# Performance work log

Hardware: AMD Instinct MI355X
Metric: run time of the kernel (lower is better)

The kernel has to match this reference:

```python
import jax, jax.numpy as jnp
import numpy as np

L = 5        # num_layer
D = 128      # emb_dim
N = 100000   # nodes
E = 500000   # edges
G = 128      # graphs in batch
NUM_TYPES = 100
NUM_ATTRS = 1000
MAX_DEPTH = 21


def _bn(x, g, b):
    # training-mode BatchNorm1d statistics (per-feature over rows)
    mu = x.mean(axis=0)
    var = x.var(axis=0)
    return (x - mu) * jax.lax.rsqrt(var + 1e-5) * g + b


def setup_inputs() -> dict:
    key = jax.random.key(0)
    ks = jax.random.split(key, 24)
    inp = {}
    x0 = jax.random.randint(ks[0], (N,), 0, NUM_TYPES)
    x1 = jax.random.randint(ks[1], (N,), 0, NUM_ATTRS)
    inp['x'] = jnp.stack([x0, x1], axis=1)
    inp['node_depth'] = jax.random.randint(ks[2], (N,), 0, MAX_DEPTH)
    inp['edge_index'] = jax.random.randint(ks[3], (2, E), 0, N)
    inp['batch'] = jnp.sort(jax.random.randint(ks[4], (N,), 0, G))
    inp['edge_attr'] = jax.random.normal(ks[5], (E, 2), dtype=jnp.float32)
    s = 0.02
    inp['type_emb'] = jax.random.normal(ks[6], (NUM_TYPES, D), dtype=jnp.float32) * s
    inp['attr_emb'] = jax.random.normal(ks[7], (NUM_ATTRS, D), dtype=jnp.float32) * s
    inp['depth_emb'] = jax.random.normal(ks[8], (MAX_DEPTH, D), dtype=jnp.float32) * s
    inp['vn_emb'] = jnp.zeros((1, D), dtype=jnp.float32)  # init constant 0
    inp['eps'] = jnp.zeros((L,), dtype=jnp.float32)       # GIN eps
    inp['edge_W'] = jax.random.normal(ks[9], (L, 2, D), dtype=jnp.float32) * s
    inp['edge_b'] = jnp.zeros((L, D), dtype=jnp.float32)
    inp['gin_W1'] = jax.random.normal(ks[10], (L, D, 2 * D), dtype=jnp.float32) * s
    inp['gin_b1'] = jnp.zeros((L, 2 * D), dtype=jnp.float32)
    inp['gin_bng'] = jnp.ones((L, 2 * D), dtype=jnp.float32)
    inp['gin_bnb'] = jnp.zeros((L, 2 * D), dtype=jnp.float32)
    inp['gin_W2'] = jax.random.normal(ks[11], (L, 2 * D, D), dtype=jnp.float32) * s
    inp['gin_b2'] = jnp.zeros((L, D), dtype=jnp.float32)
    inp['bng'] = jnp.ones((L, D), dtype=jnp.float32)
    inp['bnb'] = jnp.zeros((L, D), dtype=jnp.float32)
    inp['vn_W1'] = jax.random.normal(ks[12], (L - 1, D, 2 * D), dtype=jnp.float32) * s
    inp['vn_b1'] = jnp.zeros((L - 1, 2 * D), dtype=jnp.float32)
    inp['vn_bn1g'] = jnp.ones((L - 1, 2 * D), dtype=jnp.float32)
    inp['vn_bn1b'] = jnp.zeros((L - 1, 2 * D), dtype=jnp.float32)
    inp['vn_W2'] = jax.random.normal(ks[13], (L - 1, 2 * D, D), dtype=jnp.float32) * s
    inp['vn_b2'] = jnp.zeros((L - 1, D), dtype=jnp.float32)
    inp['vn_bn2g'] = jnp.ones((L - 1, D), dtype=jnp.float32)
    inp['vn_bn2b'] = jnp.zeros((L - 1, D), dtype=jnp.float32)
    return inp


def reference(x, node_depth, edge_index, batch, edge_attr,
              type_emb, attr_emb, depth_emb, vn_emb, eps,
              edge_W, edge_b, gin_W1, gin_b1, gin_bng, gin_bnb, gin_W2, gin_b2,
              bng, bnb, vn_W1, vn_b1, vn_bn1g, vn_bn1b, vn_W2, vn_b2, vn_bn2g, vn_bn2b):
    # node encoder: type + attribute + depth embeddings  -> [N, D]
    h = type_emb[x[:, 0]] + attr_emb[x[:, 1]] + depth_emb[node_depth]
    vn = jnp.broadcast_to(vn_emb[0], (G, D))  # virtual node per graph
    src, dst = edge_index[0], edge_index[1]
    for l in range(L):
        # broadcast virtual node to its graph's nodes
        h = h + vn[batch]
        # GIN conv: aggr_j relu(h_j + edge_emb), then (1+eps)*h + aggr -> MLP
        eemb = edge_attr @ edge_W[l] + edge_b[l]            # [E, D]
        msg = jax.nn.relu(h[src] + eemb)                    # [E, D]
        aggr = jax.ops.segment_sum(msg, dst, num_segments=N)
        z = (1.0 + eps[l]) * h + aggr
        z = jax.nn.relu(_bn(z @ gin_W1[l] + gin_b1[l], gin_bng[l], gin_bnb[l]))
        z = z @ gin_W2[l] + gin_b2[l]
        hn = _bn(z, bng[l], bnb[l])                         # outer BatchNorm
        if l < L - 1:
            hn = jax.nn.relu(hn)                            # dropout=identity (eval)
            # virtual node update: global_add_pool of pre-conv h + MLP
            vt = jax.ops.segment_sum(h, batch, num_segments=G) + vn
            vt = jax.nn.relu(_bn(vt @ vn_W1[l] + vn_b1[l], vn_bn1g[l], vn_bn1b[l]))
            vn = jax.nn.relu(_bn(vt @ vn_W2[l] + vn_b2[l], vn_bn2g[l], vn_bn2b[l]))
        h = hn
    return h  # JK == 'last'
```

## Files before the change

### kernel.cpp

```cpp
#include <hip/hip_runtime.h>

#define D 128
#define GG 128
#define SLOTS 64

typedef __attribute__((ext_vector_type(8))) short bf16x8;
typedef __attribute__((ext_vector_type(4))) float f32x4;

__device__ __forceinline__ short f2bf(float f) {
  unsigned u = __float_as_uint(f);
  unsigned r = u + 0x7fffu + ((u >> 16) & 1u);
  return (short)(r >> 16);
}
__device__ __forceinline__ float bf2f(unsigned short h) {
  return __uint_as_float(((unsigned)h) << 16);
}

__device__ __forceinline__ void bn_coef(float s, float q, float invn, float g, float b,
                                        float& sc, float& sh) {
  float mu = s * invn;
  float var = q * invn - mu * mu;
  sc = g * rsqrtf(var + 1e-5f);
  sh = b - mu * sc;
}

__global__ void k_deg(int E, const int* __restrict__ dst, int* __restrict__ deg) {
  int e = blockIdx.x * 256 + threadIdx.x;
  if (e < E) atomicAdd(&deg[dst[e]], 1);
}

__global__ void k_scan1(int N, const int* __restrict__ deg,
                        int* __restrict__ incl, int* __restrict__ blksum) {
  __shared__ int s[256];
  int t = threadIdx.x, n = blockIdx.x * 256 + t;
  int v = (n < N) ? ((deg[n] + 3) & ~3) : 0;
  s[t] = v; __syncthreads();
  for (int off = 1; off < 256; off <<= 1) {
    int x = (t >= off) ? s[t - off] : 0;
    __syncthreads();
    s[t] += x;
    __syncthreads();
  }
  if (n < N) incl[n] = s[t];
  if (t == 255) blksum[blockIdx.x] = s[255];
}

__global__ void k_scan2(int B, int* __restrict__ blksum) {
  __shared__ int s[512];
  int t = threadIdx.x;
  s[t] = (t < B) ? blksum[t] : 0;
  __syncthreads();
  for (int off = 1; off < 512; off <<= 1) {
    int x = (t >= off) ? s[t - off] : 0;
    __syncthreads();
    s[t] += x;
    __syncthreads();
  }
  if (t < B) blksum[t] = s[t];
}

__global__ void k_scan3(int N, const int* __restrict__ incl, const int* __restrict__ blksum,
                        const int* __restrict__ deg, int* __restrict__ row_ptr) {
  int n = blockIdx.x * 256 + threadIdx.x;
  if (n >= N) return;
  int b = n >> 8;
  int off = (b > 0) ? blksum[b - 1] : 0;
  int pdeg = (deg[n] + 3) & ~3;
  row_ptr[n] = off + incl[n] - pdeg;
  if (n == N - 1) row_ptr[N] = off + incl[n];
}

__global__ void k_fill(int E, const int* __restrict__ src, const int* __restrict__ dst,
                       const float* __restrict__ ea, const int* __restrict__ row_ptr,
                       int* __restrict__ cursor, int4* __restrict__ er) {
  int e = blockIdx.x * 256 + threadIdx.x;
  if (e >= E) return;
  int d = dst[e];
  int pos = row_ptr[d] + atomicAdd(&cursor[d], 1);
  er[pos] = make_int4(src[e] << 8, __float_as_int(ea[2 * e]), __float_as_int(ea[2 * e + 1]), 0);
}

__global__ void k_padfill(int N, const int* __restrict__ deg, const int* __restrict__ row_ptr,
                          int4* __restrict__ er) {
  int n = blockIdx.x * 256 + threadIdx.x;
  if (n >= N) return;
  int s = row_ptr[n] + deg[n], e = row_ptr[n + 1];
  int4 pad = make_int4(N << 8, 0, 0, 0);
  for (int p = s; p < e; ++p) er[p] = pad;
}

__global__ void k_sentinel(int N, short* __restrict__ h2) {
  h2[(size_t)N * D + threadIdx.x] = f2bf(-1e30f);
}

__global__ void k_pack(const float* __restrict__ gW1, const float* __restrict__ gW2,
                       short* __restrict__ w1t, short* __restrict__ w2t) {
  int id = blockIdx.x * 256 + threadIdx.x;
  if (id < 5 * 256 * 128) {
    int l = id / 32768, r = id % 32768, n = r / 128, k = r % 128;
    w1t[id] = f2bf(gW1[l * 32768 + k * 256 + n]);
  }
  if (id < 5 * 128 * 256) {
    int l = id / 32768, r = id % 32768, n = r / 256, k = r % 256;
    w2t[id] = f2bf(gW2[l * 32768 + k * 128 + n]);
  }
}

__global__ void k_coef(int NC,
                       const float* __restrict__ part_s, const float* __restrict__ part_q,
                       float* __restrict__ outs, float* __restrict__ outq) {
  int t = threadIdx.x;
  if (t >= NC) return;
  float s = 0.f, q = 0.f;
  #pragma unroll 4
  for (int i = 0; i < SLOTS; ++i) {
    s += part_s[i * NC + t];
    q += part_q[i * NC + t];
  }
  outs[t] = s; outq[t] = q;
}

__global__ void k_nodeprep(int N, int mode,
    const int* __restrict__ x, const int* __restrict__ depth,
    const float* __restrict__ te, const float* __restrict__ ae, const float* __restrict__ de,
    const short* __restrict__ z2, const float* __restrict__ s2, const float* __restrict__ q2,
    const float* __restrict__ g2, const float* __restrict__ b2,
    int vn_mode, const float* __restrict__ vne,
    const float* __restrict__ t2v, const float* __restrict__ vs2, const float* __restrict__ vq2,
    const float* __restrict__ vg2, const float* __restrict__ vb2,
    const int* __restrict__ batch,
    short* __restrict__ h2, float* __restrict__ vt_pool, int do_pool)
{
  int t = threadIdx.x;
  int d = t & (D - 1);
  int lane = t >> 7;
  int n0 = blockIdx.x * 16;
  float invn = 1.0f / (float)N;
  float sc = 0.f, sh = 0.f, vsc = 0.f, vsh = 0.f;
  if (mode == 1)    bn_coef(s2[d], q2[d], invn, g2[d], b2[d], sc, sh);
  if (vn_mode == 1) bn_coef(vs2[d], vq2[d], 1.0f / (float)GG, vg2[d], vb2[d], vsc, vsh);
  int cur = -1; float acc = 0.f;
  for (int k = 0; k < 8; ++k) {
    int n = n0 + lane * 8 + k;
    if (n >= N) break;
    float hv;
    if (mode == 0) {
      hv = te[x[2 * n] * D + d] + ae[x[2 * n + 1] * D + d] + de[depth[n] * D + d];
    } else {
      float z = bf2f((unsigned short)z2[(size_t)n * D + d]);
      hv = fmaxf(z * sc + sh, 0.f);
    }
    int g = batch[n];
    float vnv;
    if (vn_mode == 0) vnv = vne[d];
    else { float tv = t2v[g * D + d]; vnv = fmaxf(tv * vsc + vsh, 0.f); }
    float h = hv + vnv;
    h2[(size_t)n * D + d] = f2bf(h);
    if (do_pool) {
      if (g != cur) {
        if (cur >= 0) atomicAdd(&vt_pool[cur * D + d], acc);
        cur = g; acc = 0.f;
      }
      acc += h;
    }
  }
  if (do_pool && cur >= 0) atomicAdd(&vt_pool[cur * D + d], acc);
}

__global__ void __launch_bounds__(256) k_gather(int N,
    const int* __restrict__ row_ptr, const int4* __restrict__ er,
    const float* __restrict__ ew, const float* __restrict__ eb,
    const float* __restrict__ epsp,
    const short* __restrict__ h2, short* __restrict__ am)
{
  int t = threadIdx.x;
  int w = t >> 6, l = t & 63;
  int n = blockIdx.x * 4 + w;
  if (n >= N) return;
  const char* h2b = (const char*)h2;
  int lb = l << 2;
  int d0 = l * 2;
  float ew00 = ew[d0], ew01 = ew[d0 + 1];
  float ew10 = ew[D + d0], ew11 = ew[D + d0 + 1];
  float eb0 = eb[d0], eb1 = eb[d0 + 1];
  float ep1 = 1.0f + epsp[0];
  unsigned hv = *(const unsigned*)(h2b + ((size_t)n << 8) + lb);
  float acc0 = ep1 * bf2f((unsigned short)(hv & 0xffff));
  float acc1 = ep1 * bf2f((unsigned short)(hv >> 16));
  int beg = row_ptr[n], end = row_ptr[n + 1];
  for (int i = beg; i < end; i += 4) {
    int4 e0 = er[i], e1 = er[i + 1], e2 = er[i + 2], e3 = er[i + 3];
    unsigned v0 = *(const unsigned*)(h2b + e0.x + lb);
    unsigned v1 = *(const unsigned*)(h2b + e1.x + lb);
    unsigned v2 = *(const unsigned*)(h2b + e2.x + lb);
    unsigned v3 = *(const unsigned*)(h2b + e3.x + lb);
    float a0x = __int_as_float(e0.y), a0y = __int_as_float(e0.z);
    float a1x = __int_as_float(e1.y), a1y = __int_as_float(e1.z);
    float a2x = __int_as_float(e2.y), a2y = __int_as_float(e2.z);
    float a3x = __int_as_float(e3.y), a3y = __int_as_float(e3.z);
    acc0 += fmaxf(bf2f((unsigned short)(v0 & 0xffff)) + a0x * ew00 + a0y * ew10 + eb0, 0.f);
    acc1 += fmaxf(bf2f((unsigned short)(v0 >> 16))    + a0x * ew01 + a0y * ew11 + eb1, 0.f);
    acc0 += fmaxf(bf2f((unsigned short)(v1 & 0xffff)) + a1x * ew00 + a1y * ew10 + eb0, 0.f);
    acc1 += fmaxf(bf2f((unsigned short)(v1 >> 16))    + a1x * ew01 + a1y * ew11 + eb1, 0.f);
    acc0 += fmaxf(bf2f((unsigned short)(v2 & 0xffff)) + a2x * ew00 + a2y * ew10 + eb0, 0.f);
    acc1 += fmaxf(bf2f((unsigned short)(v2 >> 16))    + a2x * ew01 + a2y * ew11 + eb1, 0.f);
    acc0 += fmaxf(bf2f((unsigned short)(v3 & 0xffff)) + a3x * ew00 + a3y * ew10 + eb0, 0.f);
    acc1 += fmaxf(bf2f((unsigned short)(v3 >> 16))    + a3x * ew01 + a3y * ew11 + eb1, 0.f);
  }
  unsigned o = ((unsigned)(unsigned short)f2bf(acc0)) |
               (((unsigned)(unsigned short)f2bf(acc1)) << 16);
  *(unsigned*)(am + (size_t)n * D + d0) = o;
}

template<int STAGES, int BN_A>
__global__ void __launch_bounds__(256, 2) k_gemm(int N, int NC, float invn,
    const short* __restrict__ A, int strideA,
    const short* __restrict__ Bt, int strideB,
    const float* __restrict__ bias,
    const float* __restrict__ pAs, const float* __restrict__ pAq,
    const float* __restrict__ g1, const float* __restrict__ b1,
    short* __restrict__ C, int strideC,
    float* __restrict__ part_s, float* __restrict__ part_q)
{
  __shared__ __align__(16) char As[32768];
  __shared__ __align__(16) char Bs[32768];
  __shared__ float scs[256], shs[256];
  __shared__ float cs[128], cq[128];
  int t = threadIdx.x;
  int m0 = blockIdx.x * 128;
  int n0 = blockIdx.y * 128;
  int w = t >> 6, l = t & 63;
  int wr = w >> 1, wc = w & 1;
  int lm = l & 15, kb = l >> 4;

  if (t < 128) { cs[t] = 0.f; cq[t] = 0.f; }
  if (BN_A) {
    float s = 0.f, q = 0.f;
    #pragma unroll 4
    for (int i = 0; i < SLOTS; ++i) {
      s += pAs[i * 256 + t];
      q += pAq[i * 256 + t];
    }
    float a, c;
    bn_coef(s, q, invn, g1[t], b1[t], a, c);
    scs[t] = a; shs[t] = c;
  }
  __syncthreads();

  f32x4 acc[4][4];
  #pragma unroll
  for (int j = 0; j < 4; ++j) {
    float bj = bias[n0 + wc * 64 + j * 16 + lm];
    #pragma unroll
    for (int i = 0; i < 4; ++i) acc[i][j] = (f32x4){bj, bj, bj, bj};
  }

  #pragma unroll
  for (int s = 0; s < STAGES; ++s) {
    if (s > 0) __syncthreads();
    #pragma unroll
    for (int r = 0; r < 8; ++r) {
      int p = (r * 256 + t) * 16;
      int row = p >> 8, c = p & 255;
      int gr = m0 + row; if (gr > N - 1) gr = N - 1;
      bf16x8 v = *(const bf16x8*)((const char*)A + (size_t)gr * strideA + s * 256 + c);
      if (BN_A) {
        int kg = s * 128 + (c >> 1);
        float4 s0 = *(const float4*)(scs + kg);
        float4 s1 = *(const float4*)(scs + kg + 4);
        float4 h0 = *(const float4*)(shs + kg);
        float4 h1 = *(const float4*)(shs + kg + 4);
        v[0] = f2bf(fmaxf(bf2f((unsigned short)v[0]) * s0.x + h0.x, 0.f));
        v[1] = f2bf(fmaxf(bf2f((unsigned short)v[1]) * s0.y + h0.y, 0.f));
        v[2] = f2bf(fmaxf(bf2f((unsigned short)v[2]) * s0.z + h0.z, 0.f));
        v[3] = f2bf(fmaxf(bf2f((unsigned short)v[3]) * s0.w + h0.w, 0.f));
        v[4] = f2bf(fmaxf(bf2f((unsigned short)v[4]) * s1.x + h1.x, 0.f));
        v[5] = f2bf(fmaxf(bf2f((unsigned short)v[5]) * s1.y + h1.y, 0.f));
        v[6] = f2bf(fmaxf(bf2f((unsigned short)v[6]) * s1.z + h1.z, 0.f));
        v[7] = f2bf(fmaxf(bf2f((unsigned short)v[7]) * s1.w + h1.w, 0.f));
      }
      *(bf16x8*)(As + row * 256 + (c ^ ((row & 7) << 4))) = v;
    }
    #pragma unroll
    for (int r = 0; r < 8; ++r) {
      int p = (r * 256 + t) * 16;
      int col = p >> 8, c = p & 255;
      bf16x8 v = *(const bf16x8*)((const char*)Bt + (size_t)(n0 + col) * strideB + s * 256 + c);
      *(bf16x8*)(Bs + col * 256 + (c ^ ((col & 7) << 4))) = v;
    }
    __syncthreads();
    #pragma unroll
    for (int ks = 0; ks < 4; ++ks) {
      int kB = ks * 64 + kb * 16;
      bf16x8 fa[4], fb[4];
      #pragma unroll
      for (int i = 0; i < 4; ++i) {
        int rl = wr * 64 + i * 16 + lm;
        fa[i] = *(const bf16x8*)(As + rl * 256 + (kB ^ ((rl & 7) << 4)));
      }
      #pragma unroll
      for (int j = 0; j < 4; ++j) {
        int cl = wc * 64 + j * 16 + lm;
        fb[j] = *(const bf16x8*)(Bs + cl * 256 + (kB ^ ((cl & 7) << 4)));
      }
      #pragma unroll
      for (int i = 0; i < 4; ++i)
        #pragma unroll
        for (int j = 0; j < 4; ++j)
          acc[i][j] = __builtin_amdgcn_mfma_f32_16x16x32_bf16(fa[i], fb[j], acc[i][j], 0, 0, 0);
    }
  }

  #pragma unroll
  for (int j = 0; j < 4; ++j) {
    int col = n0 + wc * 64 + j * 16 + lm;
    float sv = 0.f, qv = 0.f;
    #pragma unroll
    for (int i = 0; i < 4; ++i) {
      #pragma unroll
      for (int r = 0; r < 4; ++r) {
        int row = m0 + wr * 64 + i * 16 + kb * 4 + r;
        float vv = acc[i][j][r];
        if (row < N) { C[(size_t)row * strideC + col] = f2bf(vv); sv += vv; qv += vv * vv; }
      }
    }
    sv += __shfl_xor(sv, 16); sv += __shfl_xor(sv, 32);
    qv += __shfl_xor(qv, 16); qv += __shfl_xor(qv, 32);
    if (l < 16) { atomicAdd(&cs[col - n0], sv); atomicAdd(&cq[col - n0], qv); }
  }
  __syncthreads();
  if (t < 128) {
    int slot = (blockIdx.x + blockIdx.y) & (SLOTS - 1);
    atomicAdd(&part_s[(size_t)slot * NC + n0 + t], cs[t]);
    atomicAdd(&part_q[(size_t)slot * NC + n0 + t], cq[t]);
  }
}

__global__ void k_vn1(const float* __restrict__ vt_pool,
    int vn_mode, const float* __restrict__ vne, const float* __restrict__ t2v,
    const float* __restrict__ vs2, const float* __restrict__ vq2,
    const float* __restrict__ vg2, const float* __restrict__ vb2,
    const float* __restrict__ W1, const float* __restrict__ b1,
    float* __restrict__ t1v, float* __restrict__ s1, float* __restrict__ q1)
{
  __shared__ float vrow[128];
  int g = blockIdx.x, t = threadIdx.x;
  if (t < 128) {
    float vnv;
    if (vn_mode == 0) vnv = vne[t];
    else {
      float sc, sh;
      bn_coef(vs2[t], vq2[t], 1.f / (float)GG, vg2[t], vb2[t], sc, sh);
      vnv = fmaxf(t2v[g * D + t] * sc + sh, 0.f);
    }
    vrow[t] = vt_pool[g * D + t] + vnv;
  }
  __syncthreads();
  float acc = b1[t];
  for (int k = 0; k < 128; ++k) acc += vrow[k] * W1[k * 256 + t];
  t1v[g * 256 + t] = acc;
  atomicAdd(&s1[t], acc);
  atomicAdd(&q1[t], acc * acc);
}

__global__ void k_vn2(const float* __restrict__ t1v,
    const float* __restrict__ s1, const float* __restrict__ q1,
    const float* __restrict__ g1, const float* __restrict__ b1bn,
    const float* __restrict__ W2, const float* __restrict__ b2,
    float* __restrict__ t2v, float* __restrict__ s2, float* __restrict__ q2)
{
  __shared__ float p[256];
  int g = blockIdx.x, t = threadIdx.x;
  for (int u = t; u < 256; u += 128) {
    float sc, sh;
    bn_coef(s1[u], q1[u], 1.f / (float)GG, g1[u], b1bn[u], sc, sh);
    p[u] = fmaxf(t1v[g * 256 + u] * sc + sh, 0.f);
  }
  __syncthreads();
  float acc = b2[t];
  for (int k = 0; k < 256; ++k) acc += p[k] * W2[k * D + t];
  t2v[g * D + t] = acc;
  atomicAdd(&s2[t], acc);
  atomicAdd(&q2[t], acc * acc);
}

__global__ void k_out(int N, const short* __restrict__ z2,
    const float* __restrict__ s2, const float* __restrict__ q2,
    const float* __restrict__ g2, const float* __restrict__ b2, float* __restrict__ out)
{
  long long idx = (long long)blockIdx.x * 256 + threadIdx.x;
  long long base = idx * 2;
  if (base >= (long long)N * D) return;
  int d = (int)(base & (D - 1));
  float invn = 1.f / (float)N;
  unsigned v = *(const unsigned*)(z2 + base);
  float sc0, sh0, sc1, sh1;
  bn_coef(s2[d], q2[d], invn, g2[d], b2[d], sc0, sh0);
  bn_coef(s2[d + 1], q2[d + 1], invn, g2[d + 1], b2[d + 1], sc1, sh1);
  out[base]     = bf2f((unsigned short)(v & 0xffff)) * sc0 + sh0;
  out[base + 1] = bf2f((unsigned short)(v >> 16))    * sc1 + sh1;
}

extern "C" void kernel_launch(void* const* d_in, const int* in_sizes, int n_in,
                              void* d_out, int out_size, void* d_ws, size_t ws_size,
                              hipStream_t stream) {
  const int*   x     = (const int*)d_in[0];
  const int*   depth = (const int*)d_in[1];
  const int*   eidx  = (const int*)d_in[2];
  const int*   batch = (const int*)d_in[3];
  const float* ea    = (const float*)d_in[4];
  const float* te    = (const float*)d_in[5];
  const float* aemb  = (const float*)d_in[6];
  const float* de    = (const float*)d_in[7];
  const float* vne   = (const float*)d_in[8];
  const float* epsp  = (const float*)d_in[9];
  const float* eW    = (const float*)d_in[10];
  const float* eb    = (const float*)d_in[11];
  const float* gW1   = (const float*)d_in[12];
  const float* gb1   = (const float*)d_in[13];
  const float* gbng  = (const float*)d_in[14];
  const float* gbnb  = (const float*)d_in[15];
  const float* gW2   = (const float*)d_in[16];
  const float* gb2   = (const float*)d_in[17];
  const float* bng   = (const float*)d_in[18];
  const float* bnb   = (const float*)d_in[19];
  const float* vW1   = (const float*)d_in[20];
  const float* vb1   = (const float*)d_in[21];
  const float* vbn1g = (const float*)d_in[22];
  const float* vbn1b = (const float*)d_in[23];
  const float* vW2   = (const float*)d_in[24];
  const float* vb2   = (const float*)d_in[25];
  const float* vbn2g = (const float*)d_in[26];
  const float* vbn2b = (const float*)d_in[27];

  int N = in_sizes[0] / 2;
  int E = in_sizes[2] / 2;
  const int* src = eidx;
  const int* dst = eidx + E;

  char* wsp = (char*)d_ws;
  auto alloc = [&](size_t bytes) -> char* {
    char* p = wsp; wsp += (bytes + 15) & ~(size_t)15; return p;
  };
  short* h2         = (short*)alloc((size_t)(N + 1) * 128 * 2);
  short* am         = (short*)alloc((size_t)N * 128 * 2);
  short* t1         = (short*)alloc((size_t)N * 256 * 2);
  short* z2         = (short*)alloc((size_t)N * 128 * 2);
  short* w1t        = (short*)alloc((size_t)5 * 256 * 128 * 2);
  short* w2t        = (short*)alloc((size_t)5 * 128 * 256 * 2);
  int*   row_ptr    = (int*)alloc((size_t)(N + 1) * 4);
  int*   incl       = (int*)alloc((size_t)N * 4);
  int*   blksum     = (int*)alloc(512 * 4);
  int4*  er         = (int4*)alloc(((size_t)E + 3 * (size_t)N + 16) * 16);
  char* zero_base = wsp;
  int*  deg    = (int*)alloc((size_t)N * 4);
  int*  cursor = (int*)alloc((size_t)N * 4);
  float* sp = (float*)wsp;
  float *p1s[5], *p1q[5], *p2s[5], *p2q[5], *s2s[5], *q2s[5];
  for (int l = 0; l < 5; ++l) {
    p1s[l]=sp; sp+=SLOTS*256; p1q[l]=sp; sp+=SLOTS*256;
    p2s[l]=sp; sp+=SLOTS*128; p2q[l]=sp; sp+=SLOTS*128;
    s2s[l]=sp; sp+=128; q2s[l]=sp; sp+=128;
  }
  float *vt[4], *t1v[4], *t2v[4], *vs1[4], *vq1[4], *vs2[4], *vq2[4];
  for (int l = 0; l < 4; ++l) {
    vt[l]=sp;  sp+=GG*D;
    t1v[l]=sp; sp+=GG*256;
    t2v[l]=sp; sp+=GG*D;
    vs1[l]=sp; sp+=256; vq1[l]=sp; sp+=256;
    vs2[l]=sp; sp+=128; vq2[l]=sp; sp+=128;
  }
  size_t zero_bytes = (size_t)((char*)sp - zero_base);
  hipMemsetAsync(zero_base, 0, zero_bytes, stream);

  int eblk = (E + 255) / 256;
  int nblk = (N + 255) / 256;
  int B = nblk;
  k_deg<<<eblk, 256, 0, stream>>>(E, dst, deg);
  k_scan1<<<nblk, 256, 0, stream>>>(N, deg, incl, blksum);
  k_scan2<<<1, 512, 0, stream>>>(B, blksum);
  k_scan3<<<nblk, 256, 0, stream>>>(N, incl, blksum, deg, row_ptr);
  k_fill<<<eblk, 256, 0, stream>>>(E, src, dst, ea, row_ptr, cursor, er);
  k_padfill<<<nblk, 256, 0, stream>>>(N, deg, row_ptr, er);
  k_sentinel<<<1, 128, 0, stream>>>(N, h2);

  k_pack<<<(5 * 256 * 128 + 255) / 256, 256, 0, stream>>>(gW1, gW2, w1t, w2t);

  int nblk_a = (N + 15) / 16;
  int nblk_gth = (N + 3) / 4;
  int nblk_m = (N + 127) / 128;
  float invn = 1.f / (float)N;

  for (int l = 0; l < 5; ++l) {
    int mode    = (l == 0) ? 0 : 1;
    int vn_mode = (l == 0) ? 0 : 1;
    int do_pool = (l < 4) ? 1 : 0;
    const float* ps2  = (l > 0) ? s2s[l-1] : s2s[0];
    const float* pq2  = (l > 0) ? q2s[l-1] : q2s[0];
    const float* pg2  = (l > 0) ? bng + (l-1)*D : bng;
    const float* pb2  = (l > 0) ? bnb + (l-1)*D : bnb;
    const float* pt2v = (l > 0) ? t2v[l-1] : t2v[0];
    const float* pvs2 = (l > 0) ? vs2[l-1] : vs2[0];
    const float* pvq2 = (l > 0) ? vq2[l-1] : vq2[0];
    const float* pvg2 = (l > 0) ? vbn2g + (l-1)*D : vbn2g;
    const float* pvb2 = (l > 0) ? vbn2b + (l-1)*D : vbn2b;

    k_nodeprep<<<nblk_a, 256, 0, stream>>>(N, mode, x, depth, te, aemb, de,
        z2, ps2, pq2, pg2, pb2,
        vn_mode, vne, pt2v, pvs2, pvq2, pvg2, pvb2,
        batch, h2, do_pool ? vt[l] : vt[0], do_pool);

    k_gather<<<nblk_gth, 256, 0, stream>>>(N, row_ptr, er,
        eW + l*2*D, eb + l*D, epsp + l, h2, am);

    k_gemm<1, 0><<<dim3(nblk_m, 2), 256, 0, stream>>>(N, 256, invn,
        am, 256, w1t + (size_t)l*256*128, 256,
        gb1 + l*256, nullptr, nullptr, nullptr, nullptr,
        t1, 256, p1s[l], p1q[l]);

    k_gemm<2, 1><<<dim3(nblk_m, 1), 256, 0, stream>>>(N, 128, invn,
        t1, 512, w2t + (size_t)l*128*256, 512,
        gb2 + l*128, p1s[l], p1q[l], gbng + l*256, gbnb + l*256,
        z2, 128, p2s[l], p2q[l]);

    k_coef<<<1, 128, 0, stream>>>(128, p2s[l], p2q[l], s2s[l], q2s[l]);

    if (l < 4) {
      k_vn1<<<GG, 256, 0, stream>>>(vt[l], vn_mode, vne, pt2v, pvs2, pvq2, pvg2, pvb2,
          vW1 + (size_t)l*128*256, vb1 + l*256, t1v[l], vs1[l], vq1[l]);
      k_vn2<<<GG, 128, 0, stream>>>(t1v[l], vs1[l], vq1[l],
          vbn1g + l*256, vbn1b + l*256,
          vW2 + (size_t)l*256*128, vb2 + l*128, t2v[l], vs2[l], vq2[l]);
    }
  }

  k_out<<<(int)(((long long)N * D / 2 + 255) / 256), 256, 0, stream>>>(N, z2, s2s[4], q2s[4],
      bng + 4*D, bnb + 4*D, (float*)d_out);
}
```

Measured before the change: 910.2 us.

## Fold BN-stat reductions into GEMM tails and fuse virtual-node MLP kernels

Adds a last-block ticket to each GEMM so the final block reduces the per-slot partial sums and writes either BN scale/shift coefficients or the summed stats. This removes the separate k_coef launch and the 64-slot reduction every GEMM2 block used to repeat in its prologue. k_vn1 and k_vn2 are merged into one kernel that uses a grid-wide spin barrier on a counter between the two layers. This cuts per-layer launches, but the spin barrier only works if all 128 blocks are co-resident, and the ticket pattern depends on fences being correct.

```diff
diff --git a/kernel.cpp b/kernel.cpp
--- a/kernel.cpp
+++ b/kernel.cpp
@@ -104,20 +104,6 @@
     int l = id / 32768, r = id % 32768, n = r / 256, k = r % 256;
     w2t[id] = f2bf(gW2[l * 32768 + k * 128 + n]);
   }
-}
-
-__global__ void k_coef(int NC,
-                       const float* __restrict__ part_s, const float* __restrict__ part_q,
-                       float* __restrict__ outs, float* __restrict__ outq) {
-  int t = threadIdx.x;
-  if (t >= NC) return;
-  float s = 0.f, q = 0.f;
-  #pragma unroll 4
-  for (int i = 0; i < SLOTS; ++i) {
-    s += part_s[i * NC + t];
-    q += part_q[i * NC + t];
-  }
-  outs[t] = s; outq[t] = q;
 }
 
 __global__ void k_nodeprep(int N, int mode,
@@ -212,20 +198,23 @@
   *(unsigned*)(am + (size_t)n * D + d0) = o;
 }
 
-template<int STAGES, int BN_A>
+template<int STAGES, int BN_A, int FINAL>
 __global__ void __launch_bounds__(256, 2) k_gemm(int N, int NC, float invn,
     const short* __restrict__ A, int strideA,
     const short* __restrict__ Bt, int strideB,
     const float* __restrict__ bias,
-    const float* __restrict__ pAs, const float* __restrict__ pAq,
-    const float* __restrict__ g1, const float* __restrict__ b1,
+    const float* __restrict__ scA, const float* __restrict__ shA,
+    const float* __restrict__ gam, const float* __restrict__ bet,
     short* __restrict__ C, int strideC,
-    float* __restrict__ part_s, float* __restrict__ part_q)
+    float* __restrict__ part_s, float* __restrict__ part_q,
+    int* __restrict__ ticket, int ntick,
+    float* __restrict__ outA, float* __restrict__ outB)
 {
   __shared__ __align__(16) char As[32768];
   __shared__ __align__(16) char Bs[32768];
   __shared__ float scs[256], shs[256];
   __shared__ float cs[128], cq[128];
+  __shared__ bool is_last;
   int t = threadIdx.x;
   int m0 = blockIdx.x * 128;
   int n0 = blockIdx.y * 128;
@@ -234,17 +223,7 @@
   int lm = l & 15, kb = l >> 4;
 
   if (t < 128) { cs[t] = 0.f; cq[t] = 0.f; }
-  if (BN_A) {
-    float s = 0.f, q = 0.f;
-    #pragma unroll 4
-    for (int i = 0; i < SLOTS; ++i) {
-      s += pAs[i * 256 + t];
-      q += pAq[i * 256 + t];
-    }
-    float a, c;
-    bn_coef(s, q, invn, g1[t], b1[t], a, c);
-    scs[t] = a; shs[t] = c;
-  }
+  if (BN_A) { scs[t] = scA[t]; shs[t] = shA[t]; }
   __syncthreads();
 
   f32x4 acc[4][4];
@@ -334,54 +313,82 @@
     atomicAdd(&part_s[(size_t)slot * NC + n0 + t], cs[t]);
     atomicAdd(&part_q[(size_t)slot * NC + n0 + t], cq[t]);
   }
-}
-
-__global__ void k_vn1(const float* __restrict__ vt_pool,
-    int vn_mode, const float* __restrict__ vne, const float* __restrict__ t2v,
-    const float* __restrict__ vs2, const float* __restrict__ vq2,
-    const float* __restrict__ vg2, const float* __restrict__ vb2,
+  if (t == 0) {
+    __threadfence();
+    int v = atomicAdd(ticket, 1);
+    is_last = (v == ntick - 1);
+  }
+  __syncthreads();
+  if (is_last && t < NC) {
+    float s = 0.f, q = 0.f;
+    #pragma unroll 4
+    for (int i = 0; i < SLOTS; ++i) {
+      s += __hip_atomic_load(&part_s[(size_t)i * NC + t], __ATOMIC_RELAXED, __HIP_MEMORY_SCOPE_AGENT);
+      q += __hip_atomic_load(&part_q[(size_t)i * NC + t], __ATOMIC_RELAXED, __HIP_MEMORY_SCOPE_AGENT);
+    }
+    if (FINAL == 1) {
+      float a, c;
+      bn_coef(s, q, invn, gam[t], bet[t], a, c);
+      outA[t] = a; outB[t] = c;
+    } else {
+      outA[t] = s; outB[t] = q;
+    }
+  }
+}
+
+__global__ void k_vn12(const float* __restrict__ vt_pool,
+    int vn_mode, const float* __restrict__ vne, const float* __restrict__ t2v_prev,
+    const float* __restrict__ pvs2, const float* __restrict__ pvq2,
+    const float* __restrict__ pvg2, const float* __restrict__ pvb2,
     const float* __restrict__ W1, const float* __restrict__ b1,
-    float* __restrict__ t1v, float* __restrict__ s1, float* __restrict__ q1)
+    const float* __restrict__ g1bn, const float* __restrict__ b1bn,
+    const float* __restrict__ W2, const float* __restrict__ b2,
+    float* __restrict__ t2v,
+    float* __restrict__ s1, float* __restrict__ q1,
+    float* __restrict__ s2, float* __restrict__ q2,
+    int* __restrict__ cnt)
 {
   __shared__ float vrow[128];
+  __shared__ float p[256];
   int g = blockIdx.x, t = threadIdx.x;
   if (t < 128) {
     float vnv;
     if (vn_mode == 0) vnv = vne[t];
     else {
       float sc, sh;
-      bn_coef(vs2[t], vq2[t], 1.f / (float)GG, vg2[t], vb2[t], sc, sh);
-      vnv = fmaxf(t2v[g * D + t] * sc + sh, 0.f);
+      bn_coef(pvs2[t], pvq2[t], 1.f / (float)GG, pvg2[t], pvb2[t], sc, sh);
+      vnv = fmaxf(t2v_prev[g * D + t] * sc + sh, 0.f);
     }
     vrow[t] = vt_pool[g * D + t] + vnv;
   }
   __syncthreads();
-  float acc = b1[t];
-  for (int k = 0; k < 128; ++k) acc += vrow[k] * W1[k * 256 + t];
-  t1v[g * 256 + t] = acc;
-  atomicAdd(&s1[t], acc);
-  atomicAdd(&q1[t], acc * acc);
-}
-
-__global__ void k_vn2(const float* __restrict__ t1v,
-    const float* __restrict__ s1, const float* __restrict__ q1,
-    const float* __restrict__ g1, const float* __restrict__ b1bn,
-    const float* __restrict__ W2, const float* __restrict__ b2,
-    float* __restrict__ t2v, float* __restrict__ s2, float* __restrict__ q2)
-{
-  __shared__ float p[256];
-  int g = blockIdx.x, t = threadIdx.x;
-  for (int u = t; u < 256; u += 128) {
+  float acc1 = b1[t];
+  for (int k = 0; k < 128; ++k) acc1 += vrow[k] * W1[k * 256 + t];
+  atomicAdd(&s1[t], acc1);
+  atomicAdd(&q1[t], acc1 * acc1);
+  __syncthreads();
+  if (t == 0) {
+    __threadfence();
+    atomicAdd(cnt, 1);
+    while (__hip_atomic_load(cnt, __ATOMIC_ACQUIRE, __HIP_MEMORY_SCOPE_AGENT) < GG)
+      __builtin_amdgcn_s_sleep(2);
+  }
+  __syncthreads();
+  {
+    float ss = __hip_atomic_load(&s1[t], __ATOMIC_RELAXED, __HIP_MEMORY_SCOPE_AGENT);
+    float qq = __hip_atomic_load(&q1[t], __ATOMIC_RELAXED, __HIP_MEMORY_SCOPE_AGENT);
     float sc, sh;
-    bn_coef(s1[u], q1[u], 1.f / (float)GG, g1[u], b1bn[u], sc, sh);
-    p[u] = fmaxf(t1v[g * 256 + u] * sc + sh, 0.f);
-  }
-  __syncthreads();
-  float acc = b2[t];
-  for (int k = 0; k < 256; ++k) acc += p[k] * W2[k * D + t];
-  t2v[g * D + t] = acc;
-  atomicAdd(&s2[t], acc);
-  atomicAdd(&q2[t], acc * acc);
+    bn_coef(ss, qq, 1.f / (float)GG, g1bn[t], b1bn[t], sc, sh);
+    p[t] = fmaxf(acc1 * sc + sh, 0.f);
+  }
+  __syncthreads();
+  if (t < 128) {
+    float acc2 = b2[t];
+    for (int k = 0; k < 256; ++k) acc2 += p[k] * W2[k * D + t];
+    t2v[g * D + t] = acc2;
+    atomicAdd(&s2[t], acc2);
+    atomicAdd(&q2[t], acc2 * acc2);
+  }
 }
 
 __global__ void k_out(int N, const short* __restrict__ z2,
@@ -452,9 +459,13 @@
   int*   incl       = (int*)alloc((size_t)N * 4);
   int*   blksum     = (int*)alloc(512 * 4);
   int4*  er         = (int4*)alloc(((size_t)E + 3 * (size_t)N + 16) * 16);
+  float* sc1        = (float*)alloc(256 * 4);
+  float* sh1        = (float*)alloc(256 * 4);
   char* zero_base = wsp;
   int*  deg    = (int*)alloc((size_t)N * 4);
   int*  cursor = (int*)alloc((size_t)N * 4);
+  int*  tick   = (int*)alloc(16 * 4);
+  int*  vncnt  = (int*)alloc(8 * 4);
   float* sp = (float*)wsp;
   float *p1s[5], *p1q[5], *p2s[5], *p2q[5], *s2s[5], *q2s[5];
   for (int l = 0; l < 5; ++l) {
@@ -462,10 +473,9 @@
     p2s[l]=sp; sp+=SLOTS*128; p2q[l]=sp; sp+=SLOTS*128;
     s2s[l]=sp; sp+=128; q2s[l]=sp; sp+=128;
   }
-  float *vt[4], *t1v[4], *t2v[4], *vs1[4], *vq1[4], *vs2[4], *vq2[4];
+  float *vt[4], *t2v[4], *vs1[4], *vq1[4], *vs2[4], *vq2[4];
   for (int l = 0; l < 4; ++l) {
     vt[l]=sp;  sp+=GG*D;
-    t1v[l]=sp; sp+=GG*256;
     t2v[l]=sp; sp+=GG*D;
     vs1[l]=sp; sp+=256; vq1[l]=sp; sp+=256;
     vs2[l]=sp; sp+=128; vq2[l]=sp; sp+=128;
@@ -513,24 +523,23 @@
     k_gather<<<nblk_gth, 256, 0, stream>>>(N, row_ptr, er,
         eW + l*2*D, eb + l*D, epsp + l, h2, am);
 
-    k_gemm<1, 0><<<dim3(nblk_m, 2), 256, 0, stream>>>(N, 256, invn,
+    k_gemm<1, 0, 1><<<dim3(nblk_m, 2), 256, 0, stream>>>(N, 256, invn,
         am, 256, w1t + (size_t)l*256*128, 256,
-        gb1 + l*256, nullptr, nullptr, nullptr, nullptr,
-        t1, 256, p1s[l], p1q[l]);
-
-    k_gemm<2, 1><<<dim3(nblk_m, 1), 256, 0, stream>>>(N, 128, invn,
+        gb1 + l*256, nullptr, nullptr, gbng + l*256, gbnb + l*256,
+        t1, 256, p1s[l], p1q[l], tick + 2*l, nblk_m * 2, sc1, sh1);
+
+    k_gemm<2, 1, 2><<<dim3(nblk_m, 1), 256, 0, stream>>>(N, 128, invn,
         t1, 512, w2t + (size_t)l*128*256, 512,
-        gb2 + l*128, p1s[l], p1q[l], gbng + l*256, gbnb + l*256,
-        z2, 128, p2s[l], p2q[l]);
-
-    k_coef<<<1, 128, 0, stream>>>(128, p2s[l], p2q[l], s2s[l], q2s[l]);
+        gb2 + l*128, sc1, sh1, nullptr, nullptr,
+        z2, 128, p2s[l], p2q[l], tick + 2*l + 1, nblk_m, s2s[l], q2s[l]);
 
     if (l < 4) {
-      k_vn1<<<GG, 256, 0, stream>>>(vt[l], vn_mode, vne, pt2v, pvs2, pvq2, pvg2, pvb2,
-          vW1 + (size_t)l*128*256, vb1 + l*256, t1v[l], vs1[l], vq1[l]);
-      k_vn2<<<GG, 128, 0, stream>>>(t1v[l], vs1[l], vq1[l],
+      k_vn12<<<GG, 256, 0, stream>>>(vt[l], vn_mode, vne, pt2v,
+          pvs2, pvq2, pvg2, pvb2,
+          vW1 + (size_t)l*128*256, vb1 + l*256,
           vbn1g + l*256, vbn1b + l*256,
-          vW2 + (size_t)l*256*128, vb2 + l*128, t2v[l], vs2[l], vq2[l]);
+          vW2 + (size_t)l*256*128, vb2 + l*128,
+          t2v[l], vs1[l], vq1[l], vs2[l], vq2[l], vncnt + l);
     }
   }
 
```

After: 1.291 ms. +41.9%, slower.

## Read GEMM B operand directly from global, drop B LDS tile, raise occupancy

Applied to the files above, without the earlier changes.

The GEMM kernel no longer stages the weight tile in shared memory. Each wave loads its B fragments straight from global memory (weights are small and likely cache-resident), which halves LDS use so launch bounds can rise from 2 to 4 blocks per SM. The BatchNorm coefficient reduction for the second GEMM moves out of every block into a separate small k_coef launch that writes scale and shift once, so blocks no longer each re-sum 64 partial slots. The trade-off is extra global/L2 traffic for repeated B reads, one additional kernel launch per layer, and possible register pressure under the tighter launch bound.

```diff
diff --git a/kernel.cpp b/kernel.cpp
--- a/kernel.cpp
+++ b/kernel.cpp
@@ -106,8 +106,10 @@
   }
 }
 
-__global__ void k_coef(int NC,
+__global__ void k_coef(int NC, float invn,
                        const float* __restrict__ part_s, const float* __restrict__ part_q,
+                       const float* __restrict__ g, const float* __restrict__ b,
+                       float* __restrict__ sc, float* __restrict__ sh,
                        float* __restrict__ outs, float* __restrict__ outq) {
   int t = threadIdx.x;
   if (t >= NC) return;
@@ -117,7 +119,12 @@
     s += part_s[i * NC + t];
     q += part_q[i * NC + t];
   }
-  outs[t] = s; outq[t] = q;
+  if (outs) { outs[t] = s; outq[t] = q; }
+  if (g) {
+    float a, c;
+    bn_coef(s, q, invn, g[t], b[t], a, c);
+    sc[t] = a; sh[t] = c;
+  }
 }
 
 __global__ void k_nodeprep(int N, int mode,
@@ -213,17 +220,15 @@
 }
 
 template<int STAGES, int BN_A>
-__global__ void __launch_bounds__(256, 2) k_gemm(int N, int NC, float invn,
+__global__ void __launch_bounds__(256, 4) k_gemm(int N, int NC,
     const short* __restrict__ A, int strideA,
     const short* __restrict__ Bt, int strideB,
     const float* __restrict__ bias,
-    const float* __restrict__ pAs, const float* __restrict__ pAq,
-    const float* __restrict__ g1, const float* __restrict__ b1,
+    const float* __restrict__ scA, const float* __restrict__ shA,
     short* __restrict__ C, int strideC,
     float* __restrict__ part_s, float* __restrict__ part_q)
 {
   __shared__ __align__(16) char As[32768];
-  __shared__ __align__(16) char Bs[32768];
   __shared__ float scs[256], shs[256];
   __shared__ float cs[128], cq[128];
   int t = threadIdx.x;
@@ -234,17 +239,7 @@
   int lm = l & 15, kb = l >> 4;
 
   if (t < 128) { cs[t] = 0.f; cq[t] = 0.f; }
-  if (BN_A) {
-    float s = 0.f, q = 0.f;
-    #pragma unroll 4
-    for (int i = 0; i < SLOTS; ++i) {
-      s += pAs[i * 256 + t];
-      q += pAq[i * 256 + t];
-    }
-    float a, c;
-    bn_coef(s, q, invn, g1[t], b1[t], a, c);
-    scs[t] = a; shs[t] = c;
-  }
+  if (BN_A) { scs[t] = scA[t]; shs[t] = shA[t]; }
   __syncthreads();
 
   f32x4 acc[4][4];
@@ -281,27 +276,20 @@
       }
       *(bf16x8*)(As + row * 256 + (c ^ ((row & 7) << 4))) = v;
     }
-    #pragma unroll
-    for (int r = 0; r < 8; ++r) {
-      int p = (r * 256 + t) * 16;
-      int col = p >> 8, c = p & 255;
-      bf16x8 v = *(const bf16x8*)((const char*)Bt + (size_t)(n0 + col) * strideB + s * 256 + c);
-      *(bf16x8*)(Bs + col * 256 + (c ^ ((col & 7) << 4))) = v;
-    }
     __syncthreads();
     #pragma unroll
     for (int ks = 0; ks < 4; ++ks) {
       int kB = ks * 64 + kb * 16;
       bf16x8 fa[4], fb[4];
       #pragma unroll
+      for (int j = 0; j < 4; ++j) {
+        int cl = n0 + wc * 64 + j * 16 + lm;
+        fb[j] = *(const bf16x8*)((const char*)Bt + (size_t)cl * strideB + s * 256 + kB);
+      }
+      #pragma unroll
       for (int i = 0; i < 4; ++i) {
         int rl = wr * 64 + i * 16 + lm;
         fa[i] = *(const bf16x8*)(As + rl * 256 + (kB ^ ((rl & 7) << 4)));
-      }
-      #pragma unroll
-      for (int j = 0; j < 4; ++j) {
-        int cl = wc * 64 + j * 16 + lm;
-        fb[j] = *(const bf16x8*)(Bs + cl * 256 + (kB ^ ((cl & 7) << 4)));
       }
       #pragma unroll
       for (int i = 0; i < 4; ++i)
@@ -452,6 +440,8 @@
   int*   incl       = (int*)alloc((size_t)N * 4);
   int*   blksum     = (int*)alloc(512 * 4);
   int4*  er         = (int4*)alloc(((size_t)E + 3 * (size_t)N + 16) * 16);
+  float* sc1        = (float*)alloc(256 * 4);
+  float* sh1        = (float*)alloc(256 * 4);
   char* zero_base = wsp;
   int*  deg    = (int*)alloc((size_t)N * 4);
   int*  cursor = (int*)alloc((size_t)N * 4);
@@ -513,17 +503,19 @@
     k_gather<<<nblk_gth, 256, 0, stream>>>(N, row_ptr, er,
         eW + l*2*D, eb + l*D, epsp + l, h2, am);
 
-    k_gemm<1, 0><<<dim3(nblk_m, 2), 256, 0, stream>>>(N, 256, invn,
+    k_gemm<1, 0><<<dim3(nblk_m, 2), 256, 0, stream>>>(N, 256,
         am, 256, w1t + (size_t)l*256*128, 256,
-        gb1 + l*256, nullptr, nullptr, nullptr, nullptr,
-        t1, 256, p1s[l], p1q[l]);
-
-    k_gemm<2, 1><<<dim3(nblk_m, 1), 256, 0, stream>>>(N, 128, invn,
+        gb1 + l*256, nullptr, nullptr, t1, 256, p1s[l], p1q[l]);
+
+    k_coef<<<1, 256, 0, stream>>>(256, invn, p1s[l], p1q[l],
+        gbng + l*256, gbnb + l*256, sc1, sh1, nullptr, nullptr);
+
+    k_gemm<2, 1><<<dim3(nblk_m, 1), 256, 0, stream>>>(N, 128,
         t1, 512, w2t + (size_t)l*128*256, 512,
-        gb2 + l*128, p1s[l], p1q[l], gbng + l*256, gbnb + l*256,
-        z2, 128, p2s[l], p2q[l]);
-
-    k_coef<<<1, 128, 0, stream>>>(128, p2s[l], p2q[l], s2s[l], q2s[l]);
+        gb2 + l*128, sc1, sh1, z2, 128, p2s[l], p2q[l]);
+
+    k_coef<<<1, 256, 0, stream>>>(128, invn, p2s[l], p2q[l],
+        nullptr, nullptr, nullptr, nullptr, s2s[l], q2s[l]);
 
     if (l < 4) {
       k_vn1<<<GG, 256, 0, stream>>>(vt[l], vn_mode, vne, pt2v, pvs2, pvq2, pvg2, pvb2,
```

Measured after the change: 977.6 us. 1.07x slower.

## Read GEMM B from global, stage C through LDS, widen nodeprep stores

Applied to the files above, without the earlier changes.

The GEMM no longer stages the weight tile in shared memory. B fragments are loaded straight from global memory (expected to hit cache) and the freed LDS lets occupancy rise to 4 blocks per CU. The output tile is now written into the reused A buffer and then stored as coalesced 16-byte rows instead of scattered 2-byte stores. The nodeprep kernel now handles two features per thread with packed 32-bit loads and stores. The risks are extra global and L2 traffic for the B fragments inside the inner loop and register pressure at the higher launch bound.

```diff
diff --git a/kernel.cpp b/kernel.cpp
--- a/kernel.cpp
+++ b/kernel.cpp
@@ -132,39 +132,64 @@
     short* __restrict__ h2, float* __restrict__ vt_pool, int do_pool)
 {
   int t = threadIdx.x;
-  int d = t & (D - 1);
-  int lane = t >> 7;
-  int n0 = blockIdx.x * 16;
+  int d0 = (t & 63) * 2;
+  int grp = t >> 6;
+  int n0 = blockIdx.x * 32 + grp * 8;
   float invn = 1.0f / (float)N;
-  float sc = 0.f, sh = 0.f, vsc = 0.f, vsh = 0.f;
-  if (mode == 1)    bn_coef(s2[d], q2[d], invn, g2[d], b2[d], sc, sh);
-  if (vn_mode == 1) bn_coef(vs2[d], vq2[d], 1.0f / (float)GG, vg2[d], vb2[d], vsc, vsh);
-  int cur = -1; float acc = 0.f;
+  float sc0 = 0.f, sh0 = 0.f, sc1 = 0.f, sh1 = 0.f;
+  float vsc0 = 0.f, vsh0 = 0.f, vsc1 = 0.f, vsh1 = 0.f;
+  if (mode == 1) {
+    bn_coef(s2[d0], q2[d0], invn, g2[d0], b2[d0], sc0, sh0);
+    bn_coef(s2[d0 + 1], q2[d0 + 1], invn, g2[d0 + 1], b2[d0 + 1], sc1, sh1);
+  }
+  if (vn_mode == 1) {
+    bn_coef(vs2[d0], vq2[d0], 1.0f / (float)GG, vg2[d0], vb2[d0], vsc0, vsh0);
+    bn_coef(vs2[d0 + 1], vq2[d0 + 1], 1.0f / (float)GG, vg2[d0 + 1], vb2[d0 + 1], vsc1, vsh1);
+  }
+  int cur = -1; float a0 = 0.f, a1 = 0.f;
   for (int k = 0; k < 8; ++k) {
-    int n = n0 + lane * 8 + k;
+    int n = n0 + k;
     if (n >= N) break;
-    float hv;
+    float h0, h1;
     if (mode == 0) {
-      hv = te[x[2 * n] * D + d] + ae[x[2 * n + 1] * D + d] + de[depth[n] * D + d];
+      int x0 = x[2 * n], x1 = x[2 * n + 1], dp = depth[n];
+      float2 e0 = *(const float2*)(te + (size_t)x0 * D + d0);
+      float2 e1 = *(const float2*)(ae + (size_t)x1 * D + d0);
+      float2 e2 = *(const float2*)(de + (size_t)dp * D + d0);
+      h0 = e0.x + e1.x + e2.x;
+      h1 = e0.y + e1.y + e2.y;
     } else {
-      float z = bf2f((unsigned short)z2[(size_t)n * D + d]);
-      hv = fmaxf(z * sc + sh, 0.f);
+      unsigned zv = *(const unsigned*)(z2 + (size_t)n * D + d0);
+      h0 = fmaxf(bf2f((unsigned short)(zv & 0xffff)) * sc0 + sh0, 0.f);
+      h1 = fmaxf(bf2f((unsigned short)(zv >> 16))    * sc1 + sh1, 0.f);
     }
     int g = batch[n];
-    float vnv;
-    if (vn_mode == 0) vnv = vne[d];
-    else { float tv = t2v[g * D + d]; vnv = fmaxf(tv * vsc + vsh, 0.f); }
-    float h = hv + vnv;
-    h2[(size_t)n * D + d] = f2bf(h);
+    float v0, v1;
+    if (vn_mode == 0) { v0 = vne[d0]; v1 = vne[d0 + 1]; }
+    else {
+      float2 tv = *(const float2*)(t2v + (size_t)g * D + d0);
+      v0 = fmaxf(tv.x * vsc0 + vsh0, 0.f);
+      v1 = fmaxf(tv.y * vsc1 + vsh1, 0.f);
+    }
+    h0 += v0; h1 += v1;
+    unsigned o = ((unsigned)(unsigned short)f2bf(h0)) |
+                 (((unsigned)(unsigned short)f2bf(h1)) << 16);
+    *(unsigned*)(h2 + (size_t)n * D + d0) = o;
     if (do_pool) {
       if (g != cur) {
-        if (cur >= 0) atomicAdd(&vt_pool[cur * D + d], acc);
-        cur = g; acc = 0.f;
-      }
-      acc += h;
-    }
-  }
-  if (do_pool && cur >= 0) atomicAdd(&vt_pool[cur * D + d], acc);
+        if (cur >= 0) {
+          atomicAdd(&vt_pool[cur * D + d0], a0);
+          atomicAdd(&vt_pool[cur * D + d0 + 1], a1);
+        }
+        cur = g; a0 = 0.f; a1 = 0.f;
+      }
+      a0 += h0; a1 += h1;
+    }
+  }
+  if (do_pool && cur >= 0) {
+    atomicAdd(&vt_pool[cur * D + d0], a0);
+    atomicAdd(&vt_pool[cur * D + d0 + 1], a1);
+  }
 }
 
 __global__ void __launch_bounds__(256) k_gather(int N,
@@ -213,17 +238,16 @@
 }
 
 template<int STAGES, int BN_A>
-__global__ void __launch_bounds__(256, 2) k_gemm(int N, int NC, float invn,
+__global__ void __launch_bounds__(256, 4) k_gemm(int N, int NC, float invn,
     const short* __restrict__ A, int strideA,
     const short* __restrict__ Bt, int strideB,
     const float* __restrict__ bias,
     const float* __restrict__ pAs, const float* __restrict__ pAq,
-    const float* __restrict__ g1, const float* __restrict__ b1,
+    const float* __restrict__ gam, const float* __restrict__ bet,
     short* __restrict__ C, int strideC,
     float* __restrict__ part_s, float* __restrict__ part_q)
 {
   __shared__ __align__(16) char As[32768];
-  __shared__ __align__(16) char Bs[32768];
   __shared__ float scs[256], shs[256];
   __shared__ float cs[128], cq[128];
   int t = threadIdx.x;
@@ -236,13 +260,13 @@
   if (t < 128) { cs[t] = 0.f; cq[t] = 0.f; }
   if (BN_A) {
     float s = 0.f, q = 0.f;
-    #pragma unroll 4
+    #pragma unroll 8
     for (int i = 0; i < SLOTS; ++i) {
       s += pAs[i * 256 + t];
       q += pAq[i * 256 + t];
     }
     float a, c;
-    bn_coef(s, q, invn, g1[t], b1[t], a, c);
+    bn_coef(s, q, invn, gam[t], bet[t], a, c);
     scs[t] = a; shs[t] = c;
   }
   __syncthreads();
@@ -281,27 +305,20 @@
       }
       *(bf16x8*)(As + row * 256 + (c ^ ((row & 7) << 4))) = v;
     }
-    #pragma unroll
-    for (int r = 0; r < 8; ++r) {
-      int p = (r * 256 + t) * 16;
-      int col = p >> 8, c = p & 255;
-      bf16x8 v = *(const bf16x8*)((const char*)Bt + (size_t)(n0 + col) * strideB + s * 256 + c);
-      *(bf16x8*)(Bs + col * 256 + (c ^ ((col & 7) << 4))) = v;
-    }
     __syncthreads();
     #pragma unroll
     for (int ks = 0; ks < 4; ++ks) {
       int kB = ks * 64 + kb * 16;
       bf16x8 fa[4], fb[4];
       #pragma unroll
+      for (int j = 0; j < 4; ++j) {
+        int cl = n0 + wc * 64 + j * 16 + lm;
+        fb[j] = *(const bf16x8*)((const char*)Bt + (size_t)cl * strideB + s * 256 + kB);
+      }
+      #pragma unroll
       for (int i = 0; i < 4; ++i) {
         int rl = wr * 64 + i * 16 + lm;
         fa[i] = *(const bf16x8*)(As + rl * 256 + (kB ^ ((rl & 7) << 4)));
-      }
-      #pragma unroll
-      for (int j = 0; j < 4; ++j) {
-        int cl = wc * 64 + j * 16 + lm;
-        fb[j] = *(const bf16x8*)(Bs + cl * 256 + (kB ^ ((cl & 7) << 4)));
       }
       #pragma unroll
       for (int i = 0; i < 4; ++i)
@@ -313,7 +330,7 @@
 
   #pragma unroll
   for (int j = 0; j < 4; ++j) {
-    int col = n0 + wc * 64 + j * 16 + lm;
+    int col = wc * 64 + j * 16 + lm;
     float sv = 0.f, qv = 0.f;
     #pragma unroll
     for (int i = 0; i < 4; ++i) {
@@ -321,18 +338,45 @@
       for (int r = 0; r < 4; ++r) {
         int row = m0 + wr * 64 + i * 16 + kb * 4 + r;
         float vv = acc[i][j][r];
-        if (row < N) { C[(size_t)row * strideC + col] = f2bf(vv); sv += vv; qv += vv * vv; }
+        if (row < N) { sv += vv; qv += vv * vv; }
       }
     }
     sv += __shfl_xor(sv, 16); sv += __shfl_xor(sv, 32);
     qv += __shfl_xor(qv, 16); qv += __shfl_xor(qv, 32);
-    if (l < 16) { atomicAdd(&cs[col - n0], sv); atomicAdd(&cq[col - n0], qv); }
+    if (l < 16) { atomicAdd(&cs[col], sv); atomicAdd(&cq[col], qv); }
   }
   __syncthreads();
   if (t < 128) {
     int slot = (blockIdx.x + blockIdx.y) & (SLOTS - 1);
     atomicAdd(&part_s[(size_t)slot * NC + n0 + t], cs[t]);
     atomicAdd(&part_q[(size_t)slot * NC + n0 + t], cq[t]);
+  }
+
+  #pragma unroll
+  for (int j = 0; j < 4; ++j) {
+    int colb = (wc * 64 + j * 16 + lm) * 2;
+    #pragma unroll
+    for (int i = 0; i < 4; ++i) {
+      int rowb = wr * 64 + i * 16 + kb * 4;
+      #pragma unroll
+      for (int r = 0; r < 4; ++r) {
+        int row = rowb + r;
+        *(short*)(As + row * 256 + (colb ^ ((row & 7) << 4))) = f2bf(acc[i][j][r]);
+      }
+    }
+  }
+  __syncthreads();
+  {
+    int tr = t >> 1, half = t & 1;
+    int grow = m0 + tr;
+    if (grow < N) {
+      #pragma unroll
+      for (int u = 0; u < 8; ++u) {
+        int off = half * 128 + u * 16;
+        bf16x8 v = *(const bf16x8*)(As + tr * 256 + (off ^ ((tr & 7) << 4)));
+        *(bf16x8*)(C + (size_t)grow * strideC + n0 + half * 64 + u * 8) = v;
+      }
+    }
   }
 }
 
@@ -486,7 +530,7 @@
 
   k_pack<<<(5 * 256 * 128 + 255) / 256, 256, 0, stream>>>(gW1, gW2, w1t, w2t);
 
-  int nblk_a = (N + 15) / 16;
+  int nblk_a = (N + 31) / 32;
   int nblk_gth = (N + 3) / 4;
   int nblk_m = (N + 127) / 128;
   float invn = 1.f / (float)N;
```

After: 987.0 us. 8.4% more time.
